# Optimization experiments

Measured on AMD Instinct MI355X. Metric: run time of the kernel, lower is better.

The kernel has to match this reference:

```python
import jax, jax.numpy as jnp
import numpy as np

C = 192
DCT = 7
EPS = 1e-5
LOW_X = [0,0,1,1,0,2,2,1,2,0,3,4,0,1,3,0,1,2,3,4,5,0,1,2,3,4,5,6,1,2,3,4]
LOW_Y = [0,1,0,1,2,0,1,2,2,3,0,0,4,3,1,5,4,3,2,1,0,6,5,4,3,2,1,0,6,5,4,3]


def _dct_basis():
    # basis[i, tx, ty] = bf(tx, ux_i, DCT) * bf(ty, vy_i, DCT)
    t = jnp.arange(DCT, dtype=jnp.float32)
    fx = jnp.array(LOW_X, dtype=jnp.float32)  # mapper scale = dct_h//7 = 1
    fy = jnp.array(LOW_Y, dtype=jnp.float32)
    def bf(freq):
        r = jnp.cos(jnp.pi * freq[:, None] * (t[None, :] + 0.5) / DCT) / jnp.sqrt(jnp.float32(DCT))
        return jnp.where(freq[:, None] == 0, r, r * jnp.sqrt(jnp.float32(2.0)))
    bx, by = bf(fx), bf(fy)  # [32, 7] each
    return bx[:, :, None] * by[:, None, :]  # [32, 7, 7]


def reference(x, wg1, bn2_g, bn2_b, bn2_m, bn2_v, wg2, bg2, beta, w1d, b1d, bn1_g, bn1_b, bn1_m, bn1_v):
    n, c, h, w = x.shape
    # gate: 1x1 conv -> BN2d (eval) -> ReLU -> global avg pool -> 1x1 conv
    g = jnp.einsum('nchw,oc->nohw', x, wg1)
    g = (g - bn2_m[None, :, None, None]) * (bn2_g / jnp.sqrt(bn2_v + EPS))[None, :, None, None] + bn2_b[None, :, None, None]
    g = jax.nn.relu(g).mean(axis=(2, 3))          # [n, 32]
    xg = g @ wg2.T + bg2                           # [n, 32]
    xg = jax.nn.relu(jnp.tanh(xg)) + beta          # gate_ac + beta
    # data-dependent channel partition from batch element 0 (torch uses .item() -> detached)
    xg0 = jax.lax.stop_gradient(xg[0])
    s = xg0.sum()
    p_mid = jnp.round(xg0[:31] / s * c)            # param[1..31]
    param = jnp.concatenate([jnp.zeros(1, jnp.float32), p_mid,
                             (jnp.float32(c) - p_mid.sum())[None]])  # [33]
    # build DCT filter: slice param[i]:param[i+1] gets basis i, later i overwrites
    ch = jnp.arange(c, dtype=jnp.float32)
    basis = _dct_basis()                           # [32, 7, 7]
    filt = jnp.zeros((c, DCT, DCT), jnp.float32)
    for i in range(32):
        m = (ch >= param[i]) & (ch < param[i + 1])
        filt = jnp.where(m[:, None, None], basis[i], filt)
    xp = x.reshape(n, c, DCT, h // DCT, DCT, w // DCT).mean(axis=(3, 5))
    y = jnp.sum(xp * filt[None], axis=(2, 3))      # [n, c] weighted spatial pooling
    # Conv1d(c, c, k=3, pad=1) on length-1 sequence: only center tap w1d[:, :, 1]
    y = y @ w1d[:, :, 1].T + b1d
    y = (y - bn1_m) * (bn1_g / jnp.sqrt(bn1_v + EPS)) + bn1_b
    y = jax.nn.relu(y)
    return x * y[:, :, None, None] + x


def setup_inputs() -> dict:
    key = jax.random.key(0)
    ks = jax.random.split(key, 16)
    n, h, w = 64, 56, 56
    return {
        'x':     jax.random.normal(ks[0], (n, C, h, w), jnp.float32),
        'wg1':   jax.random.normal(ks[1], (32, C), jnp.float32) * (2.0 / C) ** 0.5,
        'bn2_g': jax.random.uniform(ks[2], (32,), jnp.float32, 0.8, 1.2),
        'bn2_b': jax.random.normal(ks[3], (32,), jnp.float32) * 0.1,
        'bn2_m': jax.random.normal(ks[4], (32,), jnp.float32) * 0.1,
        'bn2_v': jax.random.uniform(ks[5], (32,), jnp.float32, 0.5, 1.5),
        'wg2':   jax.random.normal(ks[6], (32, 32), jnp.float32) * (2.0 / 32) ** 0.5,
        'bg2':   jax.random.normal(ks[7], (32,), jnp.float32) * 0.1,
        'beta':  jax.random.uniform(ks[8], (1,), jnp.float32, 0.05, 0.25),
        'w1d':   jax.random.normal(ks[9], (C, C, 3), jnp.float32) * (2.0 / (3 * C)) ** 0.5,
        'b1d':   jax.random.normal(ks[10], (C,), jnp.float32) * 0.1,
        'bn1_g': jax.random.uniform(ks[11], (C,), jnp.float32, 0.8, 1.2),
        'bn1_b': jax.random.normal(ks[12], (C,), jnp.float32) * 0.1,
        'bn1_m': jax.random.normal(ks[13], (C,), jnp.float32) * 0.1,
        'bn1_v': jax.random.uniform(ks[14], (C,), jnp.float32, 0.5, 1.5),
    }
```

## Files before the change

### kernel.cpp

```cpp
#include <hip/hip_runtime.h>
#include <hip/hip_bf16.h>
#include <math.h>

#define CCH 192
#define EPS 1e-5f

__device__ __constant__ int d_LOWX[32] = {0,0,1,1,0,2,2,1,2,0,3,4,0,1,3,0,1,2,3,4,5,0,1,2,3,4,5,6,1,2,3,4};
__device__ __constant__ int d_LOWY[32] = {0,1,0,1,2,0,1,2,2,3,0,0,4,3,1,5,4,3,2,1,0,6,5,4,3,2,1,0,6,5,4,3};

__global__ __launch_bounds__(256) void pack_wt_kernel(
    const float* __restrict__ w1d, float* __restrict__ wt) {
  const int i = blockIdx.x * 256 + threadIdx.x;
  const int c = i / CCH, k = i - c * CCH;
  wt[k * CCH + c] = w1d[c * (CCH * 3) + 3 * k + 1];
}

__global__ __launch_bounds__(256) void gate_conv_kernel(
    const float* __restrict__ x, const float* __restrict__ wg1,
    const float* __restrict__ bn2_g, const float* __restrict__ bn2_b,
    const float* __restrict__ bn2_m, const float* __restrict__ bn2_v,
    float* __restrict__ partial) {
  __shared__ float gbuf[4][32][64];
  const int h = blockIdx.x;
  const int t = threadIdx.x;
  const int cq = t >> 6;
  const int w  = t & 63;
  float acc[32];
#pragma unroll
  for (int o = 0; o < 32; ++o) acc[o] = 0.f;
  const float* xrow = x + h * 56;
  for (int c = cq * 48; c < cq * 48 + 48; ++c) {
    float xv = (w < 56) ? xrow[c * 3136 + w] : 0.f;
#pragma unroll
    for (int o = 0; o < 32; ++o) acc[o] += xv * wg1[o * 192 + c];
  }
#pragma unroll
  for (int o = 0; o < 32; ++o) gbuf[cq][o][w] = acc[o];
  __syncthreads();
  for (int e = t; e < 32 * 56; e += 256) {
    int o = e / 56, ww = e % 56;
    float v = gbuf[0][o][ww] + gbuf[1][o][ww] + gbuf[2][o][ww] + gbuf[3][o][ww];
    float sc = bn2_g[o] * rsqrtf(bn2_v[o] + EPS);
    v = v * sc + (bn2_b[o] - bn2_m[o] * sc);
    gbuf[0][o][ww] = fmaxf(v, 0.f);
  }
  __syncthreads();
  if (t < 32) {
    float s = 0.f;
    for (int ww = 0; ww < 56; ++ww) s += gbuf[0][t][ww];
    partial[h * 32 + t] = s;
  }
}

__global__ __launch_bounds__(256) void mid_kernel(
    const float* __restrict__ partial, const float* __restrict__ wg2,
    const float* __restrict__ bg2, const float* __restrict__ beta,
    float* __restrict__ filt) {
  __shared__ float gm[32];
  __shared__ float xg[32];
  __shared__ float param[33];
  __shared__ float Btab[7][7];
  const int t = threadIdx.x;
  if (t < 32) {
    float s = 0.f;
    for (int hh = 0; hh < 56; ++hh) s += partial[hh * 32 + t];
    gm[t] = s * (1.f / 3136.f);
  }
  if (t < 49) {
    int f = t / 7, tt = t % 7;
    float r = cosf(3.14159265358979323846f * (float)f * ((float)tt + 0.5f) / 7.f) * rsqrtf(7.f);
    Btab[f][tt] = (f == 0) ? r : r * sqrtf(2.f);
  }
  __syncthreads();
  if (t < 32) {
    float a = bg2[t];
    for (int k = 0; k < 32; ++k) a += gm[k] * wg2[t * 32 + k];
    xg[t] = fmaxf(tanhf(a), 0.f) + beta[0];
  }
  __syncthreads();
  if (t == 0) {
    float s = 0.f;
    for (int k = 0; k < 32; ++k) s += xg[k];
    float psum = 0.f;
    param[0] = 0.f;
    for (int i = 0; i < 31; ++i) {
      float p = rintf(xg[i] / s * (float)CCH);
      param[i + 1] = p;
      psum += p;
    }
    param[32] = (float)CCH - psum;
  }
  __syncthreads();
  for (int c = t; c < CCH; c += 256) {
    int bi = -1;
    float cf = (float)c;
    for (int i = 0; i < 32; ++i)
      if (cf >= param[i] && cf < param[i + 1]) bi = i;
    int fx = (bi >= 0) ? d_LOWX[bi] : 0;
    int fy = (bi >= 0) ? d_LOWY[bi] : 0;
    for (int cell = 0; cell < 49; ++cell) {
      int a = cell / 7, b = cell % 7;
      float v = (bi >= 0) ? Btab[fx][a] * Btab[fy][b] : 0.f;
      filt[c * 49 + cell] = v;
    }
  }
}

__global__ __launch_bounds__(256) void pool_kernel(
    const float* __restrict__ x, const float* __restrict__ filt,
    float* __restrict__ yvec) {
  __shared__ float fl[4 * 49];
  const int blk = blockIdx.x;
  const int n = blk / 48, g = blk % 48;
  const int t = threadIdx.x, wv = t >> 6, lane = t & 63;
  const int c0 = g * 4;
  if (t < 196) fl[t] = filt[c0 * 49 + t];
  __syncthreads();
  const int c = c0 + wv;
  const float4* xp = (const float4*)(x + (size_t)(n * CCH + c) * 3136);
  float acc = 0.f;
#pragma unroll
  for (int it = 0; it < 13; ++it) {
    int f = it * 64 + lane;
    if (f < 784) {
      float4 v = xp[f];
      int hh = f / 14;
      int wq = f - hh * 14;
      int cell = (hh >> 3) * 7 + (wq >> 1);
      acc += (v.x + v.y + v.z + v.w) * fl[wv * 49 + cell];
    }
  }
  acc *= (1.f / 64.f);
#pragma unroll
  for (int d = 32; d > 0; d >>= 1) acc += __shfl_xor(acc, d, 64);
  if (lane == 0) yvec[n * CCH + c] = acc;
}

__global__ __launch_bounds__(256) void out_scale_kernel(
    const float* __restrict__ yvec, const float* __restrict__ wt,
    const float* __restrict__ b1d, const float* __restrict__ bn1_g,
    const float* __restrict__ bn1_b, const float* __restrict__ bn1_m,
    const float* __restrict__ bn1_v, float* __restrict__ scale) {
  __shared__ float yl[CCH];
  const int n = blockIdx.x, t = threadIdx.x;
  if (t < CCH) yl[t] = yvec[n * CCH + t];
  __syncthreads();
  if (t < CCH) {
    float acc = b1d[t];
    for (int k = 0; k < CCH; ++k) acc += yl[k] * wt[k * CCH + t];
    float sc = bn1_g[t] * rsqrtf(bn1_v[t] + EPS);
    float v = (acc - bn1_m[t]) * sc + bn1_b[t];
    scale[n * CCH + t] = 1.f + fmaxf(v, 0.f);
  }
}

__global__ __launch_bounds__(256) void apply_kernel(
    const float* __restrict__ x, const float* __restrict__ scale,
    float* __restrict__ out) {
  const int f = blockIdx.x * 256 + threadIdx.x;
  const int nc = f / 784;
  const float s = scale[nc];
  float4 v = ((const float4*)x)[f];
  v.x *= s; v.y *= s; v.z *= s; v.w *= s;
  ((float4*)out)[f] = v;
}

extern "C" void kernel_launch(void* const* d_in, const int* in_sizes, int n_in,
                              void* d_out, int out_size, void* d_ws, size_t ws_size,
                              hipStream_t stream) {
  const float* x     = (const float*)d_in[0];
  const float* wg1   = (const float*)d_in[1];
  const float* bn2_g = (const float*)d_in[2];
  const float* bn2_b = (const float*)d_in[3];
  const float* bn2_m = (const float*)d_in[4];
  const float* bn2_v = (const float*)d_in[5];
  const float* wg2   = (const float*)d_in[6];
  const float* bg2   = (const float*)d_in[7];
  const float* beta  = (const float*)d_in[8];
  const float* w1d   = (const float*)d_in[9];
  const float* b1d   = (const float*)d_in[10];
  const float* bn1_g = (const float*)d_in[11];
  const float* bn1_b = (const float*)d_in[12];
  const float* bn1_m = (const float*)d_in[13];
  const float* bn1_v = (const float*)d_in[14];
  float* out = (float*)d_out;

  float* ws      = (float*)d_ws;
  float* partial = ws;
  float* filt    = partial + 1792;
  float* wt      = filt + 9408;
  float* yvec    = wt + 36864;
  float* scale   = yvec + 12288;

  pack_wt_kernel<<<144, 256, 0, stream>>>(w1d, wt);
  gate_conv_kernel<<<56, 256, 0, stream>>>(x, wg1, bn2_g, bn2_b, bn2_m, bn2_v, partial);
  mid_kernel<<<1, 256, 0, stream>>>(partial, wg2, bg2, beta, filt);
  pool_kernel<<<64 * 48, 256, 0, stream>>>(x, filt, yvec);
  out_scale_kernel<<<64, 256, 0, stream>>>(yvec, wt, b1d, bn1_g, bn1_b, bn1_m, bn1_v, scale);
  apply_kernel<<<37632, 256, 0, stream>>>(x, scale, out);
}
```

Before: 361.5 us.

## Fuse adaptive pooling with gate conv and weight pack into one pre-pass kernel

The 7x7 adaptive average pool, which does not depend on the gate, now runs in the same launch as the gate conv and the weight transpose, each taking its own range of blocks. Its pooled output goes to workspace, so the gate-dependent filter dot product moves into the small gemv kernel. This removes the serial dependency that forced a full second read of x after the single-block mid kernel, and cuts two launches. The pooling now accumulates with shared-memory atomics and needs an extra workspace buffer, and the apply kernel switches to nontemporal loads and stores.

```diff
diff --git a/kernel.cpp b/kernel.cpp
--- a/kernel.cpp
+++ b/kernel.cpp
@@ -5,50 +5,74 @@
 #define CCH 192
 #define EPS 1e-5f
 
+typedef float vfloat4 __attribute__((ext_vector_type(4)));
+
 __device__ __constant__ int d_LOWX[32] = {0,0,1,1,0,2,2,1,2,0,3,4,0,1,3,0,1,2,3,4,5,0,1,2,3,4,5,6,1,2,3,4};
 __device__ __constant__ int d_LOWY[32] = {0,1,0,1,2,0,1,2,2,3,0,0,4,3,1,5,4,3,2,1,0,6,5,4,3,2,1,0,6,5,4,3};
 
-__global__ __launch_bounds__(256) void pack_wt_kernel(
-    const float* __restrict__ w1d, float* __restrict__ wt) {
-  const int i = blockIdx.x * 256 + threadIdx.x;
-  const int c = i / CCH, k = i - c * CCH;
-  wt[k * CCH + c] = w1d[c * (CCH * 3) + 3 * k + 1];
-}
-
-__global__ __launch_bounds__(256) void gate_conv_kernel(
-    const float* __restrict__ x, const float* __restrict__ wg1,
+__global__ __launch_bounds__(256) void fused_pre_kernel(
+    const float* __restrict__ x, const float* __restrict__ w1d,
+    const float* __restrict__ wg1,
     const float* __restrict__ bn2_g, const float* __restrict__ bn2_b,
     const float* __restrict__ bn2_m, const float* __restrict__ bn2_v,
-    float* __restrict__ partial) {
-  __shared__ float gbuf[4][32][64];
-  const int h = blockIdx.x;
+    float* __restrict__ xp, float* __restrict__ wt, float* __restrict__ partial) {
+  __shared__ float smem[4 * 32 * 64];
+  const int b = blockIdx.x;
   const int t = threadIdx.x;
-  const int cq = t >> 6;
-  const int w  = t & 63;
-  float acc[32];
-#pragma unroll
-  for (int o = 0; o < 32; ++o) acc[o] = 0.f;
-  const float* xrow = x + h * 56;
-  for (int c = cq * 48; c < cq * 48 + 48; ++c) {
-    float xv = (w < 56) ? xrow[c * 3136 + w] : 0.f;
-#pragma unroll
-    for (int o = 0; o < 32; ++o) acc[o] += xv * wg1[o * 192 + c];
-  }
-#pragma unroll
-  for (int o = 0; o < 32; ++o) gbuf[cq][o][w] = acc[o];
-  __syncthreads();
-  for (int e = t; e < 32 * 56; e += 256) {
-    int o = e / 56, ww = e % 56;
-    float v = gbuf[0][o][ww] + gbuf[1][o][ww] + gbuf[2][o][ww] + gbuf[3][o][ww];
-    float sc = bn2_g[o] * rsqrtf(bn2_v[o] + EPS);
-    v = v * sc + (bn2_b[o] - bn2_m[o] * sc);
-    gbuf[0][o][ww] = fmaxf(v, 0.f);
-  }
-  __syncthreads();
-  if (t < 32) {
-    float s = 0.f;
-    for (int ww = 0; ww < 56; ++ww) s += gbuf[0][t][ww];
-    partial[h * 32 + t] = s;
+  if (b < 3072) {
+    const int n = b / 48, g = b % 48;
+    const int wv = t >> 6, lane = t & 63;
+    const int c0 = g * 4, c = c0 + wv;
+    if (t < 196) smem[t] = 0.f;
+    __syncthreads();
+    const vfloat4* xv = (const vfloat4*)(x + (size_t)(n * CCH + c) * 3136);
+#pragma unroll
+    for (int it = 0; it < 13; ++it) {
+      int f = it * 64 + lane;
+      if (f < 784) {
+        vfloat4 v = xv[f];
+        int hh = f / 14;
+        int wq = f - hh * 14;
+        int cell = (hh >> 3) * 7 + (wq >> 1);
+        atomicAdd(&smem[wv * 49 + cell], v.x + v.y + v.z + v.w);
+      }
+    }
+    __syncthreads();
+    if (t < 196) xp[((size_t)n * CCH + c0) * 49 + t] = smem[t] * (1.f / 64.f);
+  } else if (b < 3216) {
+    const int i = (b - 3072) * 256 + t;
+    const int c = i / CCH, k = i - c * CCH;
+    wt[k * CCH + c] = w1d[c * (CCH * 3) + 3 * k + 1];
+  } else {
+    const int h = b - 3216;
+    const int cq = t >> 6;
+    const int w  = t & 63;
+    float acc[32];
+#pragma unroll
+    for (int o = 0; o < 32; ++o) acc[o] = 0.f;
+    const float* xrow = x + h * 56;
+    for (int c = cq * 48; c < cq * 48 + 48; ++c) {
+      float xvv = (w < 56) ? xrow[c * 3136 + w] : 0.f;
+#pragma unroll
+      for (int o = 0; o < 32; ++o) acc[o] += xvv * wg1[o * 192 + c];
+    }
+#pragma unroll
+    for (int o = 0; o < 32; ++o) smem[(cq * 32 + o) * 64 + w] = acc[o];
+    __syncthreads();
+    for (int e = t; e < 32 * 56; e += 256) {
+      int o = e / 56, ww = e % 56;
+      float v = smem[(0 * 32 + o) * 64 + ww] + smem[(1 * 32 + o) * 64 + ww] +
+                smem[(2 * 32 + o) * 64 + ww] + smem[(3 * 32 + o) * 64 + ww];
+      float sc = bn2_g[o] * rsqrtf(bn2_v[o] + EPS);
+      v = v * sc + (bn2_b[o] - bn2_m[o] * sc);
+      smem[o * 64 + ww] = fmaxf(v, 0.f);
+    }
+    __syncthreads();
+    if (t < 32) {
+      float s = 0.f;
+      for (int ww = 0; ww < 56; ++ww) s += smem[t * 64 + ww];
+      partial[h * 32 + t] = s;
+    }
   }
 }
 
@@ -99,51 +123,29 @@
     int fx = (bi >= 0) ? d_LOWX[bi] : 0;
     int fy = (bi >= 0) ? d_LOWY[bi] : 0;
     for (int cell = 0; cell < 49; ++cell) {
-      int a = cell / 7, b = cell % 7;
-      float v = (bi >= 0) ? Btab[fx][a] * Btab[fy][b] : 0.f;
+      int a = cell / 7, bb = cell % 7;
+      float v = (bi >= 0) ? Btab[fx][a] * Btab[fy][bb] : 0.f;
       filt[c * 49 + cell] = v;
     }
   }
 }
 
-__global__ __launch_bounds__(256) void pool_kernel(
-    const float* __restrict__ x, const float* __restrict__ filt,
-    float* __restrict__ yvec) {
-  __shared__ float fl[4 * 49];
-  const int blk = blockIdx.x;
-  const int n = blk / 48, g = blk % 48;
-  const int t = threadIdx.x, wv = t >> 6, lane = t & 63;
-  const int c0 = g * 4;
-  if (t < 196) fl[t] = filt[c0 * 49 + t];
-  __syncthreads();
-  const int c = c0 + wv;
-  const float4* xp = (const float4*)(x + (size_t)(n * CCH + c) * 3136);
-  float acc = 0.f;
-#pragma unroll
-  for (int it = 0; it < 13; ++it) {
-    int f = it * 64 + lane;
-    if (f < 784) {
-      float4 v = xp[f];
-      int hh = f / 14;
-      int wq = f - hh * 14;
-      int cell = (hh >> 3) * 7 + (wq >> 1);
-      acc += (v.x + v.y + v.z + v.w) * fl[wv * 49 + cell];
-    }
-  }
-  acc *= (1.f / 64.f);
-#pragma unroll
-  for (int d = 32; d > 0; d >>= 1) acc += __shfl_xor(acc, d, 64);
-  if (lane == 0) yvec[n * CCH + c] = acc;
-}
-
-__global__ __launch_bounds__(256) void out_scale_kernel(
-    const float* __restrict__ yvec, const float* __restrict__ wt,
-    const float* __restrict__ b1d, const float* __restrict__ bn1_g,
-    const float* __restrict__ bn1_b, const float* __restrict__ bn1_m,
-    const float* __restrict__ bn1_v, float* __restrict__ scale) {
+__global__ __launch_bounds__(256) void gemv_scale_kernel(
+    const float* __restrict__ xp, const float* __restrict__ filt,
+    const float* __restrict__ wt, const float* __restrict__ b1d,
+    const float* __restrict__ bn1_g, const float* __restrict__ bn1_b,
+    const float* __restrict__ bn1_m, const float* __restrict__ bn1_v,
+    float* __restrict__ scale) {
   __shared__ float yl[CCH];
   const int n = blockIdx.x, t = threadIdx.x;
-  if (t < CCH) yl[t] = yvec[n * CCH + t];
+  if (t < CCH) {
+    const float* xc = xp + ((size_t)n * CCH + t) * 49;
+    const float* fc = filt + t * 49;
+    float s = 0.f;
+#pragma unroll
+    for (int cell = 0; cell < 49; ++cell) s += xc[cell] * fc[cell];
+    yl[t] = s;
+  }
   __syncthreads();
   if (t < CCH) {
     float acc = b1d[t];
@@ -160,9 +162,9 @@
   const int f = blockIdx.x * 256 + threadIdx.x;
   const int nc = f / 784;
   const float s = scale[nc];
-  float4 v = ((const float4*)x)[f];
-  v.x *= s; v.y *= s; v.z *= s; v.w *= s;
-  ((float4*)out)[f] = v;
+  vfloat4 v = __builtin_nontemporal_load(((const vfloat4*)x) + f);
+  v *= s;
+  __builtin_nontemporal_store(v, ((vfloat4*)out) + f);
 }
 
 extern "C" void kernel_launch(void* const* d_in, const int* in_sizes, int n_in,
@@ -189,13 +191,12 @@
   float* partial = ws;
   float* filt    = partial + 1792;
   float* wt      = filt + 9408;
-  float* yvec    = wt + 36864;
-  float* scale   = yvec + 12288;
-
-  pack_wt_kernel<<<144, 256, 0, stream>>>(w1d, wt);
-  gate_conv_kernel<<<56, 256, 0, stream>>>(x, wg1, bn2_g, bn2_b, bn2_m, bn2_v, partial);
+  float* xp      = wt + 36864;
+  float* scale   = xp + 602112;
+
+  fused_pre_kernel<<<3272, 256, 0, stream>>>(x, w1d, wg1, bn2_g, bn2_b, bn2_m, bn2_v,
+                                             xp, wt, partial);
   mid_kernel<<<1, 256, 0, stream>>>(partial, wg2, bg2, beta, filt);
-  pool_kernel<<<64 * 48, 256, 0, stream>>>(x, filt, yvec);
-  out_scale_kernel<<<64, 256, 0, stream>>>(yvec, wt, b1d, bn1_g, bn1_b, bn1_m, bn1_v, scale);
+  gemv_scale_kernel<<<64, 256, 0, stream>>>(xp, filt, wt, b1d, bn1_g, bn1_b, bn1_m, bn1_v, scale);
   apply_kernel<<<37632, 256, 0, stream>>>(x, scale, out);
 }
```

Measured after the change: 358.5 us. About the same (-0.8%).
